# Kernel tuning notes

Measured on AMD Instinct MI355X. Metric: run time of the kernel, lower is better.

The kernel has to match this reference:

```python
import jax, jax.numpy as jnp
import numpy as np

C = 256
GROUPS = 32
HEADS = 4
EPS = 1e-5

def setup_inputs() -> dict:
    key = jax.random.key(0)
    ks = jax.random.split(key, 6)
    N, H, W = 4, 64, 64
    s = 1.0 / np.sqrt(C)
    return {
        "x": jax.random.normal(ks[0], (N, C, H, W), dtype=jnp.float32),
        "gamma": jnp.ones((C,), jnp.float32),
        "beta": jnp.zeros((C,), jnp.float32),
        "Wq": jax.random.normal(ks[1], (C, C), jnp.float32) * s,
        "Wk": jax.random.normal(ks[2], (C, C), jnp.float32) * s,
        "Wv": jax.random.normal(ks[3], (C, C), jnp.float32) * s,
        "Wp": jax.random.normal(ks[4], (C, C), jnp.float32) * s,
        "bp": jnp.zeros((C,), jnp.float32),
    }

def group_norm(x, gamma, beta):
    N, Cc, H, W = x.shape
    xg = x.reshape(N, GROUPS, Cc // GROUPS, H, W)
    mean = jnp.mean(xg, axis=(2, 3, 4), keepdims=True)
    var = jnp.var(xg, axis=(2, 3, 4), keepdims=True)
    xg = (xg - mean) * jax.lax.rsqrt(var + EPS)
    x = xg.reshape(N, Cc, H, W)
    return x * gamma[None, :, None, None] + beta[None, :, None, None]

def reference(x, gamma, beta, Wq, Wk, Wv, Wp, bp):
    N, Cc, H, W = x.shape
    dh = Cc // HEADS
    L = H * W
    xn = group_norm(x, gamma, beta)           # [N,C,H,W]
    xf = xn.reshape(N, Cc, L)                 # [N,C,L]
    # 1x1 convs == channel matmuls; split into heads: [N,heads,L,dh]
    def proj_heads(Wm):
        t = jnp.einsum('oc,ncl->nol', Wm, xf)
        return t.reshape(N, HEADS, dh, L).transpose(0, 1, 3, 2)
    q = proj_heads(Wq)
    k = proj_heads(Wk)
    v = proj_heads(Wv)
    scale = dh ** -0.5
    attn = jnp.einsum('nhld,nhmd->nhlm', q, k) * scale  # [N,heads,L,L]
    attn = jax.nn.softmax(attn, axis=-1)
    out = jnp.einsum('nhlm,nhmd->nhld', attn, v)        # [N,heads,L,dh]
    out = out.transpose(0, 1, 3, 2).reshape(N, Cc, L)   # [N,C,L]
    out = jnp.einsum('oc,ncl->nol', Wp, out) + bp[None, :, None]
    return out.reshape(N, Cc, H, W)
```

## Files before the change

kernel.cpp:

```cpp
#include <hip/hip_runtime.h>
#include <cstddef>
#include <cstdint>

#define NB 4
#define CC 256
#define LL 4096
#define NG 32
#define CPG 8
#define NH 4
#define DH 64
#define PSPLIT 4194304

static constexpr float EPSV  = 1e-5f;
static constexpr float SCALE_Q = 0.125f * 1.4426950408889634f;

typedef __attribute__((ext_vector_type(8))) short bf16x8;
typedef __attribute__((ext_vector_type(4))) float f32x4;
typedef _Float16 f16x8 __attribute__((ext_vector_type(8)));
typedef _Float16 f16x4 __attribute__((ext_vector_type(4)));
typedef __fp16  h16x2 __attribute__((ext_vector_type(2)));

__device__ __forceinline__ short f2bf(float f) {
  unsigned u = __float_as_uint(f);
  unsigned r = (u + 0x7fffu + ((u >> 16) & 1u)) >> 16;
  return (short)r;
}
__device__ __forceinline__ short f2h(float f) {
  union { _Float16 h; short s; } u;
  u.h = (_Float16)f;
  return u.s;
}
__device__ __forceinline__ int sw(int row, int chunk) {
  return row * 64 + ((chunk ^ (row & 7)) * 8);
}

__global__ __launch_bounds__(256) void wcvt_kernel(
    const float* __restrict__ Wq, const float* __restrict__ Wk,
    const float* __restrict__ Wv, const float* __restrict__ Wp,
    short* __restrict__ dst) {
  const int which = blockIdx.x >> 5;
  const float* src = (which == 0) ? Wq : (which == 1) ? Wk : (which == 2) ? Wv : Wp;
  const int base = (blockIdx.x & 31) * 2048 + threadIdx.x * 8;
  const float4 v0 = *(const float4*)(src + base);
  const float4 v1 = *(const float4*)(src + base + 4);
  short ob[8] __attribute__((aligned(16)));
  if (which < 3) {
    ob[0] = f2bf(v0.x); ob[1] = f2bf(v0.y); ob[2] = f2bf(v0.z); ob[3] = f2bf(v0.w);
    ob[4] = f2bf(v1.x); ob[5] = f2bf(v1.y); ob[6] = f2bf(v1.z); ob[7] = f2bf(v1.w);
  } else {
    ob[0] = f2h(v0.x); ob[1] = f2h(v0.y); ob[2] = f2h(v0.z); ob[3] = f2h(v0.w);
    ob[4] = f2h(v1.x); ob[5] = f2h(v1.y); ob[6] = f2h(v1.z); ob[7] = f2h(v1.w);
  }
  *(uint4*)(dst + which * 65536 + base) = *(const uint4*)ob;
}

__global__ __launch_bounds__(256) void gn_kernel(
    const float* __restrict__ x, const float* __restrict__ gamma,
    const float* __restrict__ beta, short* __restrict__ xnT) {
  const int blk = blockIdx.x;
  const int n = blk >> 5, g = blk & 31;
  const size_t base = ((size_t)n * CC + (size_t)g * CPG) * LL;
  const float* xp = x + base;
  const int NE = CPG * LL;

  float s = 0.f, ss = 0.f;
  for (int i = threadIdx.x * 4; i < NE; i += 256 * 4) {
    float4 v = *(const float4*)(xp + i);
    s  += v.x + v.y + v.z + v.w;
    ss += v.x * v.x + v.y * v.y + v.z * v.z + v.w * v.w;
  }
  #pragma unroll
  for (int off = 32; off; off >>= 1) {
    s  += __shfl_down(s, off);
    ss += __shfl_down(ss, off);
  }
  __shared__ float r1[4], r2[4], stat[2];
  const int wid = threadIdx.x >> 6, lane = threadIdx.x & 63;
  if (lane == 0) { r1[wid] = s; r2[wid] = ss; }
  __syncthreads();
  if (threadIdx.x == 0) {
    float S = 0.f, SS = 0.f;
    #pragma unroll
    for (int w = 0; w < 4; ++w) { S += r1[w]; SS += r2[w]; }
    float mean = S / NE;
    float var  = SS / NE - mean * mean;
    stat[0] = mean;
    stat[1] = rsqrtf(var + EPSV);
  }
  __syncthreads();
  const float mean = stat[0], rstd = stat[1];
  float scl[8], shf[8];
  #pragma unroll
  for (int cc = 0; cc < 8; ++cc) {
    const float gm = gamma[g * CPG + cc];
    scl[cc] = rstd * gm;
    shf[cc] = beta[g * CPG + cc] - mean * rstd * gm;
  }
  for (int j = 0; j < 4; ++j) {
    const int l = j * 1024 + threadIdx.x * 4;
    float4 vv[8];
    #pragma unroll
    for (int cc = 0; cc < 8; ++cc)
      vv[cc] = *(const float4*)(xp + (size_t)cc * LL + l);
    short ob[4][8] __attribute__((aligned(16)));
    #pragma unroll
    for (int cc = 0; cc < 8; ++cc) {
      ob[0][cc] = f2bf(vv[cc].x * scl[cc] + shf[cc]);
      ob[1][cc] = f2bf(vv[cc].y * scl[cc] + shf[cc]);
      ob[2][cc] = f2bf(vv[cc].z * scl[cc] + shf[cc]);
      ob[3][cc] = f2bf(vv[cc].w * scl[cc] + shf[cc]);
    }
    short* op = xnT + ((size_t)n * LL + l) * CC + g * CPG;
    #pragma unroll
    for (int ii = 0; ii < 4; ++ii)
      *(uint4*)(op + (size_t)ii * CC) = *(const uint4*)ob[ii];
  }
}

__global__ __launch_bounds__(256) void qkv_gemm(
    const short* __restrict__ xnT, const short* __restrict__ Wqb,
    const short* __restrict__ Wkb, const short* __restrict__ Wvb,
    short* __restrict__ Qt, short* __restrict__ Kt, _Float16* __restrict__ Vo) {
  const int lt = blockIdx.x, ot = blockIdx.y;
  const int n = lt >> 6, l0 = (lt & 63) << 6;
  const int wave = threadIdx.x >> 6, lane = threadIdx.x & 63;
  const int lq = lane & 15, quad = lane >> 4;

  const int orow = ot * 64 + wave * 16 + lq;
  const short* wqp = Wqb + orow * CC + quad * 8;
  const short* wkp = Wkb + orow * CC + quad * 8;
  const short* wvp = Wvb + orow * CC + quad * 8;
  const short* xp  = xnT + ((size_t)(n * LL + l0) + lq) * CC + quad * 8;

  const f32x4 z = {0.f, 0.f, 0.f, 0.f};
  f32x4 aq[4] = {z, z, z, z}, ak[4] = {z, z, z, z}, av[4] = {z, z, z, z};

  #pragma unroll
  for (int c0 = 0; c0 < 256; c0 += 32) {
    const bf16x8 fq = *(const bf16x8*)(wqp + c0);
    const bf16x8 fk = *(const bf16x8*)(wkp + c0);
    const bf16x8 fv = *(const bf16x8*)(wvp + c0);
    #pragma unroll
    for (int n0 = 0; n0 < 4; ++n0) {
      const bf16x8 fb = *(const bf16x8*)(xp + (size_t)(n0 * 16) * CC + c0);
      aq[n0] = __builtin_amdgcn_mfma_f32_16x16x32_bf16(fq, fb, aq[n0], 0, 0, 0);
      ak[n0] = __builtin_amdgcn_mfma_f32_16x16x32_bf16(fk, fb, ak[n0], 0, 0, 0);
      av[n0] = __builtin_amdgcn_mfma_f32_16x16x32_bf16(fv, fb, av[n0], 0, 0, 0);
    }
  }

  const size_t hb = (size_t)(n * NH + ot);
  #pragma unroll
  for (int n0 = 0; n0 < 4; ++n0)
    #pragma unroll
    for (int r = 0; r < 4; ++r)
      Vo[(hb * DH + wave * 16 + quad * 4 + r) * LL + l0 + n0 * 16 + lq] =
          (_Float16)av[n0][r];
  __shared__ short qt_lds[64][72], kt_lds[64][72];
  #pragma unroll
  for (int n0 = 0; n0 < 4; ++n0)
    #pragma unroll
    for (int r = 0; r < 4; ++r) {
      qt_lds[n0 * 16 + lq][wave * 16 + quad * 4 + r] = f2bf(aq[n0][r] * SCALE_Q);
      kt_lds[n0 * 16 + lq][wave * 16 + quad * 4 + r] = f2bf(ak[n0][r]);
    }
  __syncthreads();
  #pragma unroll
  for (int i = 0; i < 2; ++i) {
    const int u = threadIdx.x + i * 256;
    const int row = u >> 3, ch = u & 7;
    *(uint4*)(Qt + (hb * LL + l0 + row) * DH + ch * 8) = *(const uint4*)&qt_lds[row][ch * 8];
    *(uint4*)(Kt + (hb * LL + l0 + row) * DH + ch * 8) = *(const uint4*)&kt_lds[row][ch * 8];
  }
}

__global__ __launch_bounds__(256, 2) void attn_mfma_kernel(
    const short* __restrict__ Qt, const short* __restrict__ Kt,
    const _Float16* __restrict__ Vb, _Float16* __restrict__ Opart,
    float* __restrict__ lpart) {
  __shared__ __align__(16) short    k_lds[2][64 * 64];
  __shared__ __align__(16) _Float16 v_lds[2][64 * 64];

  const int t = threadIdx.x;
  const int wave = t >> 6, lane = t & 63;
  const int lq = lane & 15, quad = lane >> 4;
  const int l0 = blockIdx.x * 256;
  const int h = blockIdx.y >> 1, split = blockIdx.y & 1;
  const int n = blockIdx.z;
  const int kbase = split * 2048;
  const int R = n * NH + h;
  const size_t hb = (size_t)R * (size_t)LL * DH;
  const short* const Kp = Kt + hb;
  const _Float16* const Vp = Vb + hb;

  const int qbase = l0 + wave * 64;
  bf16x8 qb[4][2];
  #pragma unroll
  for (int qf = 0; qf < 4; ++qf)
    #pragma unroll
    for (int c = 0; c < 2; ++c)
      qb[qf][c] = *(const bf16x8*)(Qt + hb + (size_t)(qbase + qf * 16 + lq) * DH + c * 32 + quad * 8);

  const f32x4 z = {0.f, 0.f, 0.f, 0.f};
  f32x4 o[4][4] = {{z, z, z, z}, {z, z, z, z}, {z, z, z, z}, {z, z, z, z}};
  f32x4 ol[4] = {z, z, z, z};

  f16x8 ones8;
  #pragma unroll
  for (int i = 0; i < 8; ++i) ones8[i] = (_Float16)1.0f;

  const int srow = t >> 3, sch = t & 7;
  const int vgo = 32 * (sch >> 2) + 4 * (sch & 3);

  {
    *(uint4*)&k_lds[0][sw(srow, sch)]      = *(const uint4*)(Kp + (size_t)(kbase + srow) * DH + sch * 8);
    *(uint4*)&k_lds[0][sw(32 + srow, sch)] = *(const uint4*)(Kp + (size_t)(kbase + 32 + srow) * DH + sch * 8);
    const _Float16* vg0 = Vp + (size_t)srow * LL + kbase + vgo;
    const _Float16* vg1 = Vp + (size_t)(32 + srow) * LL + kbase + vgo;
    uint2 a = *(const uint2*)vg0, b = *(const uint2*)(vg0 + 16);
    *(uint4*)&v_lds[0][sw(srow, sch)] = make_uint4(a.x, a.y, b.x, b.y);
    a = *(const uint2*)vg1; b = *(const uint2*)(vg1 + 16);
    *(uint4*)&v_lds[0][sw(32 + srow, sch)] = make_uint4(a.x, a.y, b.x, b.y);
  }
  __syncthreads();

  for (int kt = 0; kt < 32; ++kt) {
    const int cur = kt & 1;
    uint4 kpre[2]; uint2 vpre[4];
    if (kt < 31) {
      const int kpos = kbase + (kt + 1) * 64;
      kpre[0] = *(const uint4*)(Kp + (size_t)(kpos + srow) * DH + sch * 8);
      kpre[1] = *(const uint4*)(Kp + (size_t)(kpos + 32 + srow) * DH + sch * 8);
      const _Float16* vg0 = Vp + (size_t)srow * LL + kpos + vgo;
      const _Float16* vg1 = Vp + (size_t)(32 + srow) * LL + kpos + vgo;
      vpre[0] = *(const uint2*)vg0;
      vpre[1] = *(const uint2*)(vg0 + 16);
      vpre[2] = *(const uint2*)vg1;
      vpre[3] = *(const uint2*)(vg1 + 16);
    }
    const short* kb = k_lds[cur];
    const _Float16* vbuf = v_lds[cur];

    union PU { f16x4 h4[2]; f16x8 h8; } af[2][4];
    #pragma unroll
    for (int mf = 0; mf < 4; ++mf) {
      const bf16x8 ka0 = *(const bf16x8*)&kb[sw(mf * 16 + lq, quad)];
      const bf16x8 ka1 = *(const bf16x8*)&kb[sw(mf * 16 + lq, 4 + quad)];
      #pragma unroll
      for (int qf = 0; qf < 4; ++qf) {
        f32x4 zz = {0.f, 0.f, 0.f, 0.f};
        zz = __builtin_amdgcn_mfma_f32_16x16x32_bf16(ka0, qb[qf][0], zz, 0, 0, 0);
        zz = __builtin_amdgcn_mfma_f32_16x16x32_bf16(ka1, qb[qf][1], zz, 0, 0, 0);
        union { h16x2 h2[2]; f16x4 h4; } u;
        u.h2[0] = __builtin_amdgcn_cvt_pkrtz(__builtin_amdgcn_exp2f(zz[0]),
                                             __builtin_amdgcn_exp2f(zz[1]));
        u.h2[1] = __builtin_amdgcn_cvt_pkrtz(__builtin_amdgcn_exp2f(zz[2]),
                                             __builtin_amdgcn_exp2f(zz[3]));
        af[mf >> 1][qf].h4[mf & 1] = u.h4;
      }
    }

    #pragma unroll
    for (int qf = 0; qf < 4; ++qf) {
      ol[qf] = __builtin_amdgcn_mfma_f32_16x16x32_f16(af[0][qf].h8, ones8, ol[qf], 0, 0, 0);
      ol[qf] = __builtin_amdgcn_mfma_f32_16x16x32_f16(af[1][qf].h8, ones8, ol[qf], 0, 0, 0);
    }

    #pragma unroll
    for (int df = 0; df < 4; ++df)
      #pragma unroll
      for (int cc = 0; cc < 2; ++cc) {
        const f16x8 vb8 = *(const f16x8*)&vbuf[sw(df * 16 + lq, cc * 4 + quad)];
        #pragma unroll
        for (int qf = 0; qf < 4; ++qf)
          o[qf][df] = __builtin_amdgcn_mfma_f32_16x16x32_f16(af[cc][qf].h8, vb8, o[qf][df], 0, 0, 0);
      }

    if (kt < 31) {
      const int nxt = 1 - cur;
      *(uint4*)&k_lds[nxt][sw(srow, sch)]      = kpre[0];
      *(uint4*)&k_lds[nxt][sw(32 + srow, sch)] = kpre[1];
      *(uint4*)&v_lds[nxt][sw(srow, sch)]      = make_uint4(vpre[0].x, vpre[0].y, vpre[1].x, vpre[1].y);
      *(uint4*)&v_lds[nxt][sw(32 + srow, sch)] = make_uint4(vpre[2].x, vpre[2].y, vpre[3].x, vpre[3].y);
      __syncthreads();
    }
  }

  const size_t pb = ((size_t)split * 16 + R) * (size_t)LL * DH;
  #pragma unroll
  for (int qf = 0; qf < 4; ++qf) {
    if (lq == 0) {
      #pragma unroll
      for (int r = 0; r < 4; ++r)
        lpart[((size_t)split * 16 + R) * LL + qbase + qf * 16 + quad * 4 + r] = ol[qf][r];
    }
    #pragma unroll
    for (int df = 0; df < 4; ++df)
      #pragma unroll
      for (int r = 0; r < 4; ++r) {
        const int q = qbase + qf * 16 + quad * 4 + r;
        Opart[pb + (size_t)q * DH + df * 16 + lq] = (_Float16)o[qf][df][r];
      }
  }
}

__global__ __launch_bounds__(256) void proj_gemm(
    const _Float16* __restrict__ Opart, const float* __restrict__ lpart,
    const _Float16* __restrict__ Wpf, const float* __restrict__ bp,
    float* __restrict__ out) {
  const int lt = blockIdx.x, ot2 = blockIdx.y;
  const int n = lt >> 6, l0 = (lt & 63) << 6;
  const int wave = threadIdx.x >> 6, lane = threadIdx.x & 63;
  const int lq = lane & 15, quad = lane >> 4;

  const _Float16* wpp0 = Wpf + (ot2 * 128 + wave * 16 + lq) * CC + quad * 8;
  const _Float16* wpp1 = wpp0 + 64 * CC;

  _Float16 invl[4][4];
  #pragma unroll
  for (int n0 = 0; n0 < 4; ++n0) {
    const int q = l0 + n0 * 16 + lq;
    #pragma unroll
    for (int h = 0; h < 4; ++h) {
      const size_t rr = (size_t)(n * NH + h) * LL + q;
      invl[n0][h] = (_Float16)(1.0f / (lpart[rr] + lpart[rr + 16 * (size_t)LL]));
    }
  }

  const f32x4 z = {0.f, 0.f, 0.f, 0.f};
  f32x4 acc[2][4] = {{z, z, z, z}, {z, z, z, z}};
  #pragma unroll
  for (int c0 = 0; c0 < 256; c0 += 32) {
    const int h = c0 >> 6;
    const int d0 = (c0 & 63) + quad * 8;
    const f16x8 fa0 = *(const f16x8*)(wpp0 + c0);
    const f16x8 fa1 = *(const f16x8*)(wpp1 + c0);
    #pragma unroll
    for (int n0 = 0; n0 < 4; ++n0) {
      const int q = l0 + n0 * 16 + lq;
      const size_t e = ((size_t)(n * NH + h) * LL + q) * DH + d0;
      const f16x8 b0 = *(const f16x8*)(Opart + e);
      const f16x8 b1 = *(const f16x8*)(Opart + e + PSPLIT);
      f16x8 sc8;
      #pragma unroll
      for (int i = 0; i < 8; ++i) sc8[i] = invl[n0][h];
      const f16x8 fb = (b0 + b1) * sc8;
      acc[0][n0] = __builtin_amdgcn_mfma_f32_16x16x32_f16(fa0, fb, acc[0][n0], 0, 0, 0);
      acc[1][n0] = __builtin_amdgcn_mfma_f32_16x16x32_f16(fa1, fb, acc[1][n0], 0, 0, 0);
    }
  }
  #pragma unroll
  for (int w = 0; w < 2; ++w)
    #pragma unroll
    for (int r = 0; r < 4; ++r) {
      const int oo = ot2 * 128 + w * 64 + wave * 16 + quad * 4 + r;
      const float bias = bp[oo];
      #pragma unroll
      for (int n0 = 0; n0 < 4; ++n0)
        out[((size_t)n * CC + oo) * LL + l0 + n0 * 16 + lq] = acc[w][n0][r] + bias;
    }
}

extern "C" void kernel_launch(void* const* d_in, const int* in_sizes, int n_in,
                              void* d_out, int out_size, void* d_ws, size_t ws_size,
                              hipStream_t stream) {
  const float* x     = (const float*)d_in[0];
  const float* gamma = (const float*)d_in[1];
  const float* beta  = (const float*)d_in[2];
  const float* Wq    = (const float*)d_in[3];
  const float* Wk    = (const float*)d_in[4];
  const float* Wv    = (const float*)d_in[5];
  const float* Wp    = (const float*)d_in[6];
  const float* bp    = (const float*)d_in[7];
  float* out = (float*)d_out;

  const size_t S = (size_t)NB * CC * LL;
  short*     xnT = (short*)d_ws;
  short*     Qt  = xnT + S;
  short*     Kt  = Qt + S;
  _Float16*  Vo  = (_Float16*)(Kt + S);
  short*     Wb  = (short*)(Vo + S);
  _Float16*  Opart = (_Float16*)(Wb + 4 * 65536);
  float*     lpart = (float*)(Opart + 2 * PSPLIT);

  gn_kernel  <<<NB * NG,              256, 0, stream>>>(x, gamma, beta, xnT);
  wcvt_kernel<<<128,                  256, 0, stream>>>(Wq, Wk, Wv, Wp, Wb);
  qkv_gemm   <<<dim3(256, 4),         256, 0, stream>>>(xnT, Wb, Wb + 65536, Wb + 131072, Qt, Kt, Vo);
  attn_mfma_kernel<<<dim3(LL/256, NH*2, NB), 256, 0, stream>>>(Qt, Kt, Vo, Opart, lpart);
  proj_gemm  <<<dim3(256, 2),         256, 0, stream>>>(Opart, lpart,
                 (const _Float16*)(Wb + 196608), bp, out);
}
```

Baseline: 211.7 us.

## Split attention keys four ways and merge GroupNorm with weight conversion

Result: slower. 482.7 us (+128.1%).

```diff
diff --git a/kernel.cpp b/kernel.cpp
--- a/kernel.cpp
+++ b/kernel.cpp
@@ -9,6 +9,7 @@
 #define CPG 8
 #define NH 4
 #define DH 64
+#define NSPLIT 4
 #define PSPLIT 4194304
 
 static constexpr float EPSV  = 1e-5f;
@@ -34,29 +35,30 @@
   return row * 64 + ((chunk ^ (row & 7)) * 8);
 }
 
-__global__ __launch_bounds__(256) void wcvt_kernel(
+__global__ __launch_bounds__(256) void gnw_kernel(
+    const float* __restrict__ x, const float* __restrict__ gamma,
+    const float* __restrict__ beta, short* __restrict__ xnT,
     const float* __restrict__ Wq, const float* __restrict__ Wk,
     const float* __restrict__ Wv, const float* __restrict__ Wp,
-    short* __restrict__ dst) {
-  const int which = blockIdx.x >> 5;
-  const float* src = (which == 0) ? Wq : (which == 1) ? Wk : (which == 2) ? Wv : Wp;
-  const int base = (blockIdx.x & 31) * 2048 + threadIdx.x * 8;
-  const float4 v0 = *(const float4*)(src + base);
-  const float4 v1 = *(const float4*)(src + base + 4);
-  short ob[8] __attribute__((aligned(16)));
-  if (which < 3) {
-    ob[0] = f2bf(v0.x); ob[1] = f2bf(v0.y); ob[2] = f2bf(v0.z); ob[3] = f2bf(v0.w);
-    ob[4] = f2bf(v1.x); ob[5] = f2bf(v1.y); ob[6] = f2bf(v1.z); ob[7] = f2bf(v1.w);
-  } else {
-    ob[0] = f2h(v0.x); ob[1] = f2h(v0.y); ob[2] = f2h(v0.z); ob[3] = f2h(v0.w);
-    ob[4] = f2h(v1.x); ob[5] = f2h(v1.y); ob[6] = f2h(v1.z); ob[7] = f2h(v1.w);
-  }
-  *(uint4*)(dst + which * 65536 + base) = *(const uint4*)ob;
-}
-
-__global__ __launch_bounds__(256) void gn_kernel(
-    const float* __restrict__ x, const float* __restrict__ gamma,
-    const float* __restrict__ beta, short* __restrict__ xnT) {
+    short* __restrict__ Wb) {
+  if (blockIdx.x >= 128) {
+    const int bb = blockIdx.x - 128;
+    const int which = bb >> 5;
+    const float* src = (which == 0) ? Wq : (which == 1) ? Wk : (which == 2) ? Wv : Wp;
+    const int base = (bb & 31) * 2048 + threadIdx.x * 8;
+    const float4 v0 = *(const float4*)(src + base);
+    const float4 v1 = *(const float4*)(src + base + 4);
+    short ob[8] __attribute__((aligned(16)));
+    if (which < 3) {
+      ob[0] = f2bf(v0.x); ob[1] = f2bf(v0.y); ob[2] = f2bf(v0.z); ob[3] = f2bf(v0.w);
+      ob[4] = f2bf(v1.x); ob[5] = f2bf(v1.y); ob[6] = f2bf(v1.z); ob[7] = f2bf(v1.w);
+    } else {
+      ob[0] = f2h(v0.x); ob[1] = f2h(v0.y); ob[2] = f2h(v0.z); ob[3] = f2h(v0.w);
+      ob[4] = f2h(v1.x); ob[5] = f2h(v1.y); ob[6] = f2h(v1.z); ob[7] = f2h(v1.w);
+    }
+    *(uint4*)(Wb + which * 65536 + base) = *(const uint4*)ob;
+    return;
+  }
   const int blk = blockIdx.x;
   const int n = blk >> 5, g = blk & 31;
   const size_t base = ((size_t)n * CC + (size_t)g * CPG) * LL;
@@ -174,7 +176,7 @@
   }
 }
 
-__global__ __launch_bounds__(256, 2) void attn_mfma_kernel(
+__global__ __launch_bounds__(256, 4) void attn_mfma_kernel(
     const short* __restrict__ Qt, const short* __restrict__ Kt,
     const _Float16* __restrict__ Vb, _Float16* __restrict__ Opart,
     float* __restrict__ lpart) {
@@ -185,9 +187,9 @@
   const int wave = t >> 6, lane = t & 63;
   const int lq = lane & 15, quad = lane >> 4;
   const int l0 = blockIdx.x * 256;
-  const int h = blockIdx.y >> 1, split = blockIdx.y & 1;
+  const int h = blockIdx.y >> 2, split = blockIdx.y & 3;
   const int n = blockIdx.z;
-  const int kbase = split * 2048;
+  const int kbase = split * 1024;
   const int R = n * NH + h;
   const size_t hb = (size_t)R * (size_t)LL * DH;
   const short* const Kp = Kt + hb;
@@ -224,10 +226,10 @@
   }
   __syncthreads();
 
-  for (int kt = 0; kt < 32; ++kt) {
+  for (int kt = 0; kt < 16; ++kt) {
     const int cur = kt & 1;
     uint4 kpre[2]; uint2 vpre[4];
-    if (kt < 31) {
+    if (kt < 15) {
       const int kpos = kbase + (kt + 1) * 64;
       kpre[0] = *(const uint4*)(Kp + (size_t)(kpos + srow) * DH + sch * 8);
       kpre[1] = *(const uint4*)(Kp + (size_t)(kpos + 32 + srow) * DH + sch * 8);
@@ -276,7 +278,7 @@
           o[qf][df] = __builtin_amdgcn_mfma_f32_16x16x32_f16(af[cc][qf].h8, vb8, o[qf][df], 0, 0, 0);
       }
 
-    if (kt < 31) {
+    if (kt < 15) {
       const int nxt = 1 - cur;
       *(uint4*)&k_lds[nxt][sw(srow, sch)]      = kpre[0];
       *(uint4*)&k_lds[nxt][sw(32 + srow, sch)] = kpre[1];
@@ -323,7 +325,10 @@
     #pragma unroll
     for (int h = 0; h < 4; ++h) {
       const size_t rr = (size_t)(n * NH + h) * LL + q;
-      invl[n0][h] = (_Float16)(1.0f / (lpart[rr] + lpart[rr + 16 * (size_t)LL]));
+      float lsum = 0.f;
+      #pragma unroll
+      for (int s = 0; s < NSPLIT; ++s) lsum += lpart[rr + (size_t)s * 16 * LL];
+      invl[n0][h] = (_Float16)(1.0f / lsum);
     }
   }
 
@@ -341,10 +346,12 @@
       const size_t e = ((size_t)(n * NH + h) * LL + q) * DH + d0;
       const f16x8 b0 = *(const f16x8*)(Opart + e);
       const f16x8 b1 = *(const f16x8*)(Opart + e + PSPLIT);
+      const f16x8 b2 = *(const f16x8*)(Opart + e + 2 * (size_t)PSPLIT);
+      const f16x8 b3 = *(const f16x8*)(Opart + e + 3 * (size_t)PSPLIT);
       f16x8 sc8;
       #pragma unroll
       for (int i = 0; i < 8; ++i) sc8[i] = invl[n0][h];
-      const f16x8 fb = (b0 + b1) * sc8;
+      const f16x8 fb = ((b0 + b1) + (b2 + b3)) * sc8;
       acc[0][n0] = __builtin_amdgcn_mfma_f32_16x16x32_f16(fa0, fb, acc[0][n0], 0, 0, 0);
       acc[1][n0] = __builtin_amdgcn_mfma_f32_16x16x32_f16(fa1, fb, acc[1][n0], 0, 0, 0);
     }
@@ -375,18 +382,18 @@
   float* out = (float*)d_out;
 
   const size_t S = (size_t)NB * CC * LL;
-  short*     xnT = (short*)d_ws;
-  short*     Qt  = xnT + S;
+  short*     Qt  = (short*)d_ws;
   short*     Kt  = Qt + S;
   _Float16*  Vo  = (_Float16*)(Kt + S);
   short*     Wb  = (short*)(Vo + S);
-  _Float16*  Opart = (_Float16*)(Wb + 4 * 65536);
-  float*     lpart = (float*)(Opart + 2 * PSPLIT);
-
-  gn_kernel  <<<NB * NG,              256, 0, stream>>>(x, gamma, beta, xnT);
-  wcvt_kernel<<<128,                  256, 0, stream>>>(Wq, Wk, Wv, Wp, Wb);
+  float*     lpart = (float*)(Wb + 4 * 65536);
+  _Float16*  Opart = (_Float16*)(lpart + NSPLIT * 16 * LL);
+  short*     xnT = (short*)Opart;
+
+  gnw_kernel <<<256,                  256, 0, stream>>>(x, gamma, beta, xnT,
+                                                        Wq, Wk, Wv, Wp, Wb);
   qkv_gemm   <<<dim3(256, 4),         256, 0, stream>>>(xnT, Wb, Wb + 65536, Wb + 131072, Qt, Kt, Vo);
-  attn_mfma_kernel<<<dim3(LL/256, NH*2, NB), 256, 0, stream>>>(Qt, Kt, Vo, Opart, lpart);
+  attn_mfma_kernel<<<dim3(LL/256, NH*NSPLIT, NB), 256, 0, stream>>>(Qt, Kt, Vo, Opart, lpart);
   proj_gemm  <<<dim3(256, 2),         256, 0, stream>>>(Opart, lpart,
                  (const _Float16*)(Wb + 196608), bp, out);
 }
```
